# Kernel optimization log

Measured on AMD Instinct MI355X. Metric: run time of the kernel, lower is better.

Reference implementation:

```python
import jax, jax.numpy as jnp
import numpy as np

B, S, F = 16, 511, 128           # batch, input seq len, n_features
D, H, NB = 512, 8, 6             # embedding_dim, n_heads, n_blocks
DH = D // H                      # d_head
MLP = 4 * D                      # mlp_ratio=4 hard-coded in FxtBlock
OUT = 1                          # out_d
T = S + 1                        # tokens incl. cls
EPS = 1e-5                       # torch LayerNorm default eps


def pos_emb(seq_len, d):
    # matches get_positional_embeddings: sin for even j, cos for odd j (with j-1 exponent)
    i = np.arange(seq_len, dtype=np.float32)[:, None]
    j = np.arange(d)
    je = np.where(j % 2 == 0, j, j - 1).astype(np.float32)
    ang = i / (10000.0 ** (je / d))
    pe = np.where(j % 2 == 0, np.sin(ang), np.cos(ang))
    return jnp.asarray(pe, jnp.float32)


def layernorm(x, g, b):
    m = jnp.mean(x, axis=-1, keepdims=True)
    v = jnp.mean((x - m) ** 2, axis=-1, keepdims=True)
    return (x - m) * jax.lax.rsqrt(v + EPS) * g + b


def setup_inputs() -> dict:
    key = jax.random.key(0)
    ks = jax.random.split(key, 12)
    g = lambda k, shape: jax.random.normal(k, shape, jnp.float32) * 0.02
    return {
        "src": jax.random.normal(ks[0], (B, S, F), jnp.float32),
        "emb_W": g(ks[1], (F, D)), "emb_b": jnp.zeros((D,), jnp.float32),
        "cls_tok": jax.random.uniform(ks[2], (1, D), jnp.float32),
        "ln1_g": jnp.ones((NB, D), jnp.float32), "ln1_b": jnp.zeros((NB, D), jnp.float32),
        "Wq": g(ks[3], (NB, H, DH, DH)), "bq": jnp.zeros((NB, H, DH), jnp.float32),
        "Wk": g(ks[4], (NB, H, DH, DH)), "bk": jnp.zeros((NB, H, DH), jnp.float32),
        "Wv": g(ks[5], (NB, H, DH, DH)), "bv": jnp.zeros((NB, H, DH), jnp.float32),
        "ln2_g": jnp.ones((NB, D), jnp.float32), "ln2_b": jnp.zeros((NB, D), jnp.float32),
        "W1": g(ks[6], (NB, D, MLP)), "b1": jnp.zeros((NB, MLP), jnp.float32),
        "W2": g(ks[7], (NB, MLP, D)), "b2": jnp.zeros((NB, D), jnp.float32),
        "head_W": g(ks[8], (D, OUT)), "head_b": jnp.zeros((OUT,), jnp.float32),
    }


def reference(src, emb_W, emb_b, cls_tok, ln1_g, ln1_b, Wq, bq, Wk, bk, Wv, bv,
              ln2_g, ln2_b, W1, b1, W2, b2, head_W, head_b):
    b = src.shape[0]
    x = src @ emb_W + emb_b                                    # [B,S,D]
    cls = jnp.broadcast_to(cls_tok[None], (b, 1, D))
    x = jnp.concatenate([cls, x], axis=1) + pos_emb(T, D)[None]  # [B,T,D]
    scale = 1.0 / jnp.sqrt(jnp.float32(DH))
    for i in range(NB):
        h = layernorm(x, ln1_g[i], ln1_b[i])
        hh = h.reshape(b, T, H, DH)
        q = jnp.einsum('bthd,hde->bhte', hh, Wq[i]) + bq[i][None, :, None, :]
        k = jnp.einsum('bthd,hde->bhte', hh, Wk[i]) + bk[i][None, :, None, :]
        v = jnp.einsum('bthd,hde->bhte', hh, Wv[i]) + bv[i][None, :, None, :]
        attn = jax.nn.softmax(jnp.einsum('bhse,bhte->bhst', q, k) * scale, axis=-1)
        o = jnp.einsum('bhst,bhte->bhse', attn, v)             # [B,H,T,DH]
        x = x + o.transpose(0, 2, 1, 3).reshape(b, T, D)
        h2 = layernorm(x, ln2_g[i], ln2_b[i])
        x = x + (jax.nn.gelu(h2 @ W1[i] + b1[i], approximate=False) @ W2[i] + b2[i])
    return jax.nn.sigmoid(x[:, 0] @ head_W + head_b)           # [B,OUT]
```

## Files before the change

kernel.cpp:

```cpp
#include <hip/hip_runtime.h>
#include <hip/hip_bf16.h>
#include <math.h>

#define B 16
#define S 511
#define F 128
#define D 512
#define H 8
#define NB 6
#define DH 64
#define MLPD 2048
#define T 512
#define EPS 1e-5f

typedef unsigned short ushort;
typedef __attribute__((ext_vector_type(8))) short short8;
typedef __attribute__((ext_vector_type(4))) float floatx4;

__device__ __forceinline__ ushort f2bf(float f) {
    union { float f; unsigned u; } cv; cv.f = f;
    unsigned r = (cv.u + 0x7fff + ((cv.u >> 16) & 1)) >> 16;
    return (ushort)r;
}

__device__ __forceinline__ float fast_gelu(float x) {
    float z = fabsf(x) * 0.70710678118f;
    float t = 1.0f / (1.0f + 0.3275911f * z);
    float p = ((((1.061405429f * t - 1.453152027f) * t + 1.421413741f) * t
               - 0.284496736f) * t + 0.254829592f) * t;
    float erfv = 1.0f - p * __expf(-z * z);
    erfv = copysignf(erfv, x);
    return 0.5f * x * (1.0f + erfv);
}

__global__ void castsrc_kernel(const float* __restrict__ src, ushort* __restrict__ srcb) {
    int row = blockIdx.x;
    int t = row & (T - 1), b = row >> 9;
    int tid = threadIdx.x;
    ushort v = 0;
    if (t > 0) v = f2bf(src[((size_t)b * S + (t - 1)) * F + tid]);
    srcb[(size_t)row * F + tid] = v;
}

__global__ void wtrans_kernel(const float* __restrict__ W,
                              ushort* __restrict__ Wt,
                              int K, int N) {
    int kb = blockIdx.x * 32, nb = blockIdx.y * 32, mat = blockIdx.z;
    __shared__ float tile[32][33];
    int tid = threadIdx.x;
    int c = tid & 31, r0 = tid >> 5;
    const float* Wm = W + (size_t)mat * K * N;
    ushort* Wtm = Wt + (size_t)mat * K * N;
    #pragma unroll
    for (int l = 0; l < 4; ++l) {
        int r = r0 + l * 8;
        tile[r][c] = Wm[(size_t)(kb + r) * N + nb + c];
    }
    __syncthreads();
    #pragma unroll
    for (int l = 0; l < 4; ++l) {
        int r = r0 + l * 8;
        Wtm[(size_t)(nb + r) * K + kb + c] = f2bf(tile[c][r]);
    }
}

__global__ void wtransq_kernel(const float* __restrict__ Wq, const float* __restrict__ Wk,
                               const float* __restrict__ Wv,
                               ushort* __restrict__ WqT, ushort* __restrict__ WkT,
                               ushort* __restrict__ WvT) {
    int mat = blockIdx.x;
    int which = blockIdx.y;
    const float* W = (which == 0 ? Wq : which == 1 ? Wk : Wv) + (size_t)mat * 4096;
    ushort* O = (which == 0 ? WqT : which == 1 ? WkT : WvT) + (size_t)mat * 4096;
    __shared__ float t[64][65];
    int tid = threadIdx.x;
    int r0 = tid >> 6, c = tid & 63;
    #pragma unroll
    for (int l = 0; l < 16; ++l) {
        int row = r0 * 16 + l;
        t[row][c] = W[row * 64 + c];
    }
    __syncthreads();
    #pragma unroll
    for (int l = 0; l < 16; ++l) {
        int row = r0 * 16 + l;
        O[row * 64 + c] = f2bf(t[c][row]);
    }
}

__device__ __forceinline__ void gload_lds16(const ushort* g, ushort* l) {
    __builtin_amdgcn_global_load_lds((const __attribute__((address_space(1))) unsigned int*)g,
                                     (__attribute__((address_space(3))) unsigned int*)l,
                                     16, 0, 0);
}

#define S_WAITCNT_VM(N) asm volatile("s_waitcnt vmcnt(" #N ")" ::: "memory")

__global__ __launch_bounds__(256) void embed_gemm(const ushort* __restrict__ A,
                                                  const ushort* __restrict__ Bt,
                                                  const float* __restrict__ emb_b,
                                                  const float* __restrict__ cls_tok,
                                                  float* __restrict__ x) {
    __shared__ ushort As[64 * 32];
    __shared__ ushort Bs[64 * 32];
    int tid = threadIdx.x;
    int lane = tid & 63;
    int w = __builtin_amdgcn_readfirstlane(tid >> 6);
    int quad = lane >> 4, l15 = lane & 15;
    int wr = (w >> 1) * 32, wc = (w & 1) * 32;
    int m0 = blockIdx.x * 64, n0 = blockIdx.y * 64;

    floatx4 acc[2][2];
    #pragma unroll
    for (int i = 0; i < 2; ++i)
        #pragma unroll
        for (int j = 0; j < 2; ++j) acc[i][j] = (floatx4)0.f;

    int lrow = lane >> 2;
    int lk = (lane & 3) * 8;
    const ushort* Ag = A + (size_t)(m0 + 16 * w + lrow) * F + lk;
    const ushort* Bg = Bt + (size_t)(n0 + 16 * w + lrow) * F + lk;
    ushort* AsW = &As[16 * w * 32];
    ushort* BsW = &Bs[16 * w * 32];
    int fa = l15 * 32 + quad * 8;

    for (int kt = 0; kt < F; kt += 32) {
        gload_lds16(Ag + kt, AsW);
        gload_lds16(Bg + kt, BsW);
        __syncthreads();
        short8 af[2], bf[2];
        #pragma unroll
        for (int i = 0; i < 2; ++i) af[i] = *(const short8*)&As[(wr + 16 * i) * 32 + fa];
        #pragma unroll
        for (int j = 0; j < 2; ++j) bf[j] = *(const short8*)&Bs[(wc + 16 * j) * 32 + fa];
        #pragma unroll
        for (int i = 0; i < 2; ++i)
            #pragma unroll
            for (int j = 0; j < 2; ++j)
                acc[i][j] = __builtin_amdgcn_mfma_f32_16x16x32_bf16(af[i], bf[j], acc[i][j], 0, 0, 0);
        __syncthreads();
    }

    const float LOG1E4 = 9.210340371976184f;
    int rbase = (lane >> 4) * 4;
    int cidx = lane & 15;
    #pragma unroll
    for (int j = 0; j < 2; ++j) {
        int gc = n0 + wc + 16 * j + cidx;
        float je = (float)(gc & ~1);
        float freq = expf(-(je / (float)D) * LOG1E4);
        float ebv = emb_b[gc];
        float clsv = cls_tok[gc];
        bool odd = (gc & 1);
        #pragma unroll
        for (int i = 0; i < 2; ++i) {
            int gr = m0 + wr + 16 * i + rbase;
            #pragma unroll
            for (int reg = 0; reg < 4; ++reg) {
                int row = gr + reg;
                int t = row & (T - 1);
                float ang = (float)t * freq;
                float pe = odd ? cosf(ang) : sinf(ang);
                float val = (t == 0) ? (clsv + pe) : (acc[i][j][reg] + ebv + pe);
                x[(size_t)row * D + gc] = val;
            }
        }
    }
}

__global__ __launch_bounds__(256) void ln_kernel(const float* __restrict__ xin,
                                                 const float* __restrict__ g,
                                                 const float* __restrict__ bb,
                                                 ushort* __restrict__ out) {
    int lane = threadIdx.x & 63;
    int row = blockIdx.x * 4 + (threadIdx.x >> 6);
    const float* xr = xin + (size_t)row * D + lane * 8;
    float4 a0 = *(const float4*)xr;
    float4 a1 = *(const float4*)(xr + 4);
    float s = a0.x + a0.y + a0.z + a0.w + a1.x + a1.y + a1.z + a1.w;
    #pragma unroll
    for (int off = 1; off < 64; off <<= 1) s += __shfl_xor(s, off);
    float mean = s * (1.0f / (float)D);
    float d0 = a0.x - mean, d1 = a0.y - mean, d2 = a0.z - mean, d3 = a0.w - mean;
    float d4 = a1.x - mean, d5 = a1.y - mean, d6 = a1.z - mean, d7 = a1.w - mean;
    float sq = d0*d0 + d1*d1 + d2*d2 + d3*d3 + d4*d4 + d5*d5 + d6*d6 + d7*d7;
    #pragma unroll
    for (int off = 1; off < 64; off <<= 1) sq += __shfl_xor(sq, off);
    float rstd = rsqrtf(sq * (1.0f / (float)D) + EPS);
    const float* gp = g + lane * 8;
    const float* bp = bb + lane * 8;
    float4 g0 = *(const float4*)gp, g1 = *(const float4*)(gp + 4);
    float4 b0 = *(const float4*)bp, b1 = *(const float4*)(bp + 4);
    short8 o;
    o[0] = (short)f2bf(d0 * rstd * g0.x + b0.x);
    o[1] = (short)f2bf(d1 * rstd * g0.y + b0.y);
    o[2] = (short)f2bf(d2 * rstd * g0.z + b0.z);
    o[3] = (short)f2bf(d3 * rstd * g0.w + b0.w);
    o[4] = (short)f2bf(d4 * rstd * g1.x + b1.x);
    o[5] = (short)f2bf(d5 * rstd * g1.y + b1.y);
    o[6] = (short)f2bf(d6 * rstd * g1.z + b1.z);
    o[7] = (short)f2bf(d7 * rstd * g1.w + b1.w);
    *(short8*)(out + (size_t)row * D + lane * 8) = o;
}

__global__ __launch_bounds__(256) void ln_fuse_kernel(float* __restrict__ x,
                                                      const float* __restrict__ p0,
                                                      const float* __restrict__ g,
                                                      const float* __restrict__ bb,
                                                      ushort* __restrict__ out) {
    int lane = threadIdx.x & 63;
    int row = blockIdx.x * 4 + (threadIdx.x >> 6);
    size_t base = (size_t)row * D + lane * 8;
    float* xr = x + base;
    float4 a0 = *(const float4*)xr;
    float4 a1 = *(const float4*)(xr + 4);
    float4 q0 = *(const float4*)(p0 + base);
    float4 q1 = *(const float4*)(p0 + base + 4);
    a0.x += q0.x; a0.y += q0.y; a0.z += q0.z; a0.w += q0.w;
    a1.x += q1.x; a1.y += q1.y; a1.z += q1.z; a1.w += q1.w;
    *(float4*)xr = a0;
    *(float4*)(xr + 4) = a1;
    float s = a0.x + a0.y + a0.z + a0.w + a1.x + a1.y + a1.z + a1.w;
    #pragma unroll
    for (int off = 1; off < 64; off <<= 1) s += __shfl_xor(s, off);
    float mean = s * (1.0f / (float)D);
    float d0 = a0.x - mean, d1 = a0.y - mean, d2 = a0.z - mean, d3 = a0.w - mean;
    float d4 = a1.x - mean, d5 = a1.y - mean, d6 = a1.z - mean, d7 = a1.w - mean;
    float sq = d0*d0 + d1*d1 + d2*d2 + d3*d3 + d4*d4 + d5*d5 + d6*d6 + d7*d7;
    #pragma unroll
    for (int off = 1; off < 64; off <<= 1) sq += __shfl_xor(sq, off);
    float rstd = rsqrtf(sq * (1.0f / (float)D) + EPS);
    const float* gp = g + lane * 8;
    const float* bp = bb + lane * 8;
    float4 g0 = *(const float4*)gp, g1 = *(const float4*)(gp + 4);
    float4 b0 = *(const float4*)bp, b1 = *(const float4*)(bp + 4);
    short8 o;
    o[0] = (short)f2bf(d0 * rstd * g0.x + b0.x);
    o[1] = (short)f2bf(d1 * rstd * g0.y + b0.y);
    o[2] = (short)f2bf(d2 * rstd * g0.z + b0.z);
    o[3] = (short)f2bf(d3 * rstd * g0.w + b0.w);
    o[4] = (short)f2bf(d4 * rstd * g1.x + b1.x);
    o[5] = (short)f2bf(d5 * rstd * g1.y + b1.y);
    o[6] = (short)f2bf(d6 * rstd * g1.z + b1.z);
    o[7] = (short)f2bf(d7 * rstd * g1.w + b1.w);
    *(short8*)(out + (size_t)row * D + lane * 8) = o;
}

__global__ __launch_bounds__(256) void qkv_kernel(
        const ushort* __restrict__ hb,
        const ushort* __restrict__ WqT, const float* __restrict__ bq,
        const ushort* __restrict__ WkT, const float* __restrict__ bk,
        const ushort* __restrict__ WvT, const float* __restrict__ bv,
        ushort* __restrict__ qo, ushort* __restrict__ ko, ushort* __restrict__ vTo) {
    int m0 = blockIdx.x * 128;
    int hh = blockIdx.y;
    int tid = threadIdx.x;
    int lane = tid & 63;
    int w = __builtin_amdgcn_readfirstlane(tid >> 6);
    int quad = lane >> 4, l15 = lane & 15;

    short8 af[2][2];
    #pragma unroll
    for (int mt = 0; mt < 2; ++mt) {
        const ushort* ab = hb + (size_t)(m0 + w * 32 + mt * 16 + l15) * D + hh * DH + quad * 8;
        af[mt][0] = *(const short8*)(ab);
        af[mt][1] = *(const short8*)(ab + 32);
    }

    floatx4 acc[3][2][4];
    #pragma unroll
    for (int xo = 0; xo < 3; ++xo)
        #pragma unroll
        for (int mt = 0; mt < 2; ++mt)
            #pragma unroll
            for (int nt = 0; nt < 4; ++nt) acc[xo][mt][nt] = (floatx4)0.f;

    #pragma unroll
    for (int xo = 0; xo < 3; ++xo) {
        const ushort* WT = (xo == 0 ? WqT : xo == 1 ? WkT : WvT) + (size_t)hh * 4096;
        #pragma unroll
        for (int nt = 0; nt < 4; ++nt) {
            const ushort* wb = WT + (size_t)(nt * 16 + l15) * 64 + quad * 8;
            short8 bf0 = *(const short8*)(wb);
            short8 bf1 = *(const short8*)(wb + 32);
            #pragma unroll
            for (int mt = 0; mt < 2; ++mt) {
                acc[xo][mt][nt] = __builtin_amdgcn_mfma_f32_16x16x32_bf16(af[mt][0], bf0, acc[xo][mt][nt], 0, 0, 0);
                acc[xo][mt][nt] = __builtin_amdgcn_mfma_f32_16x16x32_bf16(af[mt][1], bf1, acc[xo][mt][nt], 0, 0, 0);
            }
        }
    }

    int bb = m0 >> 9;
    int bh = bb * H + hh;
    #pragma unroll
    for (int mt = 0; mt < 2; ++mt) {
        int trow = m0 + w * 32 + mt * 16 + quad * 4;
        int tt = trow & (T - 1);
        #pragma unroll
        for (int nt = 0; nt < 4; ++nt) {
            int col = nt * 16 + l15;
            float bqv = bq[hh * DH + col];
            float bkv = bk[hh * DH + col];
            float bvv = bv[hh * DH + col];
            #pragma unroll
            for (int reg = 0; reg < 4; ++reg) {
                qo[((size_t)bh * T + tt + reg) * DH + col] = f2bf(acc[0][mt][nt][reg] + bqv);
                ko[((size_t)bh * T + tt + reg) * DH + col] = f2bf(acc[1][mt][nt][reg] + bkv);
                vTo[((size_t)bh * DH + col) * T + tt + reg] = f2bf(acc[2][mt][nt][reg] + bvv);
            }
        }
    }
}

#define PSTRIDE 88
__global__ __launch_bounds__(256) void attn_kernel(const ushort* __restrict__ q,
                                                   const ushort* __restrict__ k,
                                                   const ushort* __restrict__ vT,
                                                   float* __restrict__ x) {
    int bh = blockIdx.x;
    int qt = blockIdx.y;
    int b = bh >> 3, hh = bh & 7;
    int tid = threadIdx.x;
    int lane = tid & 63;
    int w = __builtin_amdgcn_readfirstlane(tid >> 6);
    int quad = lane >> 4, l15 = lane & 15;

    __shared__ __align__(16) ushort smem[22016];
    ushort* Pw = smem + 16384 + w * (16 * PSTRIDE);

    const ushort* qbase = q + ((size_t)bh * T + qt * 64 + w * 16 + l15) * DH + quad * 8;
    short8 Qf0 = *(const short8*)(qbase);
    short8 Qf1 = *(const short8*)(qbase + 32);

    const ushort* kbase = k + (size_t)bh * T * DH;
    const ushort* vbase = vT + (size_t)bh * DH * T;

    int srow = lane >> 2;
    int scol = (lane & 3) * 8;
    const ushort* kg = kbase + (size_t)(w * 16 + srow) * DH + scol;
    const ushort* vg = vbase + (size_t)(w * 16 + srow) * T + scol;
    ushort* ldsK = smem + w * 16 * 32;
    ushort* ldsV = smem + 8192 + w * 16 * 32;

    float l_i[4] = {0.f, 0.f, 0.f, 0.f};
    floatx4 O[4];
    #pragma unroll
    for (int j = 0; j < 4; ++j) O[j] = (floatx4)0.f;

    gload_lds16(kg, ldsK);
    gload_lds16(kg + 32, ldsK + 2048);
    gload_lds16(vg, ldsV);
    gload_lds16(vg + 32, ldsV + 2048);
    __syncthreads();

    for (int kt = 0; kt < T / 64; ++kt) {
        int cur = kt & 1;
        if (kt < T / 64 - 1) {
            int nb = cur ^ 1;
            const ushort* kgn = kg + (size_t)(kt + 1) * 64 * DH;
            const ushort* vgn = vg + (kt + 1) * 64;
            gload_lds16(kgn, ldsK + nb * 4096);
            gload_lds16(kgn + 32, ldsK + nb * 4096 + 2048);
            gload_lds16(vgn, ldsV + nb * 4096);
            gload_lds16(vgn + 32, ldsV + nb * 4096 + 2048);
        }
        const ushort* Kc = smem + cur * 4096;
        const ushort* Vc = smem + 8192 + cur * 4096;

        floatx4 sc[4];
        #pragma unroll
        for (int j = 0; j < 4; ++j) {
            int ro = (j * 16 + l15) * 32 + quad * 8;
            short8 kf0 = *(const short8*)&Kc[ro];
            short8 kf1 = *(const short8*)&Kc[2048 + ro];
            floatx4 s4 = (floatx4)0.f;
            s4 = __builtin_amdgcn_mfma_f32_16x16x32_bf16(Qf0, kf0, s4, 0, 0, 0);
            s4 = __builtin_amdgcn_mfma_f32_16x16x32_bf16(Qf1, kf1, s4, 0, 0, 0);
            sc[j] = s4;
        }
        #pragma unroll
        for (int j = 0; j < 4; ++j) {
            #pragma unroll
            for (int r = 0; r < 4; ++r) {
                float p = __expf(sc[j][r] * 0.125f);
                l_i[r] += p;
                Pw[(quad * 4 + r) * PSTRIDE + j * 16 + l15] = f2bf(p);
            }
        }

        short8 af0 = *(const short8*)&Pw[l15 * PSTRIDE + quad * 8];
        short8 af1 = *(const short8*)&Pw[l15 * PSTRIDE + 32 + quad * 8];
        #pragma unroll
        for (int j = 0; j < 4; ++j) {
            int ro = (j * 16 + l15) * 32 + quad * 8;
            short8 vf0 = *(const short8*)&Vc[ro];
            short8 vf1 = *(const short8*)&Vc[2048 + ro];
            O[j] = __builtin_amdgcn_mfma_f32_16x16x32_bf16(af0, vf0, O[j], 0, 0, 0);
            O[j] = __builtin_amdgcn_mfma_f32_16x16x32_bf16(af1, vf1, O[j], 0, 0, 0);
        }
        __syncthreads();
    }

    #pragma unroll
    for (int r = 0; r < 4; ++r) {
        l_i[r] += __shfl_xor(l_i[r], 1);
        l_i[r] += __shfl_xor(l_i[r], 2);
        l_i[r] += __shfl_xor(l_i[r], 4);
        l_i[r] += __shfl_xor(l_i[r], 8);
    }

    float* Ow = (float*)smem + w * 16 * 68;
    #pragma unroll
    for (int r = 0; r < 4; ++r) {
        float rl = 1.0f / l_i[r];
        #pragma unroll
        for (int j = 0; j < 4; ++j)
            Ow[(quad * 4 + r) * 68 + j * 16 + l15] = O[j][r] * rl;
    }
    __syncthreads();
    int r4 = lane >> 4;
    int c16 = lane & 15;
    #pragma unroll
    for (int i = 0; i < 4; ++i) {
        int lrow = i * 4 + r4;
        float4 o = *(const float4*)&Ow[lrow * 68 + c16 * 4];
        int grow = qt * 64 + w * 16 + lrow;
        float* xp = &x[((size_t)(b * T) + grow) * D + hh * DH + c16 * 4];
        float4 xv = *(const float4*)xp;
        xv.x += o.x; xv.y += o.y; xv.z += o.z; xv.w += o.w;
        *(float4*)xp = xv;
    }
}

template<int BM, int EPI>
__global__ __launch_bounds__(512) void gemm_pipe(const ushort* __restrict__ A,
                                                 const ushort* __restrict__ Bt,
                                                 const float* __restrict__ bias,
                                                 void* __restrict__ Cout,
                                                 int N, int K) {
    constexpr int BN = 128;
    constexpr int BK = 64;
    constexpr int MREP = BM / 32;
    constexpr int AJ = BM / 64;
    constexpr int TILE = (BM + BN) * BK;
    __shared__ ushort lds[3 * TILE];

    int tid = threadIdx.x;
    int lane = tid & 63;
    int w = __builtin_amdgcn_readfirstlane(tid >> 6);
    int quad = lane >> 4, l15 = lane & 15;
    int wrow = (w >> 2) * (BM / 2);
    int wcol = (w & 3) * 32;
    int m0 = blockIdx.x * BM, n0 = blockIdx.y * BN;

    int lrow8 = lane >> 3;
    int lslot = lane & 7;
    int scol = (lslot ^ lrow8) * 8;
    const ushort* Asrc = A + (size_t)(m0 + w * 8 + lrow8) * K + scol;
    const ushort* Bsrc = Bt + (size_t)(n0 + w * 8 + lrow8) * K + scol;
    ushort* ldsA0 = lds + (w * 8) * BK;
    ushort* ldsB0 = lds + BM * BK + (w * 8) * BK;

    int sx0 = ((quad) ^ (l15 & 7)) * 8;
    int sx1 = ((4 + quad) ^ (l15 & 7)) * 8;

    floatx4 acc[MREP][2];
    #pragma unroll
    for (int i = 0; i < MREP; ++i) {
        acc[i][0] = (floatx4)0.f;
        acc[i][1] = (floatx4)0.f;
    }

    #define STAGE_T(t, buf) do {                                                   \
        const ushort* ap_ = Asrc + (size_t)(t) * BK;                               \
        const ushort* bp_ = Bsrc + (size_t)(t) * BK;                               \
        ushort* la_ = ldsA0 + (buf) * TILE;                                        \
        ushort* lb_ = ldsB0 + (buf) * TILE;                                        \
        _Pragma("unroll")                                                          \
        for (int j = 0; j < AJ; ++j)                                               \
            gload_lds16(ap_ + (size_t)j * 64 * K, la_ + j * 64 * BK);              \
        _Pragma("unroll")                                                          \
        for (int j = 0; j < 2; ++j)                                                \
            gload_lds16(bp_ + (size_t)j * 64 * K, lb_ + j * 64 * BK);              \
    } while (0)

    #define COMPUTE_T(buf) do {                                                    \
        const ushort* Ab_ = lds + (buf) * TILE;                                    \
        const ushort* Bb_ = Ab_ + BM * BK;                                         \
        _Pragma("unroll")                                                          \
        for (int ks = 0; ks < 2; ++ks) {                                           \
            int sx_ = ks ? sx1 : sx0;                                              \
            short8 bfr0 = *(const short8*)&Bb_[(wcol + l15) * BK + sx_];           \
            short8 bfr1 = *(const short8*)&Bb_[(wcol + 16 + l15) * BK + sx_];      \
            _Pragma("unroll")                                                      \
            for (int i = 0; i < MREP; ++i) {                                       \
                short8 af_ = *(const short8*)&Ab_[(wrow + i * 16 + l15) * BK + sx_]; \
                acc[i][0] = __builtin_amdgcn_mfma_f32_16x16x32_bf16(af_, bfr0, acc[i][0], 0, 0, 0); \
                acc[i][1] = __builtin_amdgcn_mfma_f32_16x16x32_bf16(af_, bfr1, acc[i][1], 0, 0, 0); \
            }                                                                      \
        }                                                                          \
    } while (0)

    STAGE_T(0, 0);
    STAGE_T(1, 1);

    int NT = K / BK;
    int cb = 0, nbuf = 2;
    for (int t = 0; t < NT - 2; ++t) {
        STAGE_T(t + 2, nbuf);
        if constexpr (AJ == 4) { S_WAITCNT_VM(12); } else { S_WAITCNT_VM(8); }
        __builtin_amdgcn_s_barrier();
        __builtin_amdgcn_s_setprio(1);
        COMPUTE_T(cb);
        __builtin_amdgcn_s_setprio(0);
        asm volatile("s_waitcnt lgkmcnt(0)" ::: "memory");
        __builtin_amdgcn_s_barrier();
        cb = (cb == 2) ? 0 : cb + 1;
        nbuf = (nbuf == 2) ? 0 : nbuf + 1;
    }
    if constexpr (AJ == 4) { S_WAITCNT_VM(6); } else { S_WAITCNT_VM(4); }
    __builtin_amdgcn_s_barrier();
    __builtin_amdgcn_s_setprio(1);
    COMPUTE_T(cb);
    __builtin_amdgcn_s_setprio(0);
    asm volatile("s_waitcnt lgkmcnt(0)" ::: "memory");
    __builtin_amdgcn_s_barrier();
    cb = (cb == 2) ? 0 : cb + 1;
    S_WAITCNT_VM(0);
    __builtin_amdgcn_s_barrier();
    COMPUTE_T(cb);

    #undef STAGE_T
    #undef COMPUTE_T

    int rbase = quad * 4;
    #pragma unroll
    for (int i = 0; i < MREP; ++i) {
        #pragma unroll
        for (int n = 0; n < 2; ++n) {
            int gc = n0 + wcol + n * 16 + l15;
            float bv = bias[gc];
            int gr = m0 + wrow + i * 16 + rbase;
            #pragma unroll
            for (int reg = 0; reg < 4; ++reg) {
                if constexpr (EPI == 0) {
                    ((ushort*)Cout)[(size_t)(gr + reg) * N + gc] =
                        f2bf(fast_gelu(acc[i][n][reg] + bv));
                } else {
                    ((float*)Cout)[(size_t)(gr + reg) * N + gc] = acc[i][n][reg] + bv;
                }
            }
        }
    }
}

__global__ __launch_bounds__(256) void ln_cls_kernel(const float* __restrict__ x,
                                                     const float* __restrict__ g,
                                                     const float* __restrict__ bb,
                                                     ushort* __restrict__ h2c) {
    int lane = threadIdx.x & 63;
    int r = blockIdx.x * 4 + (threadIdx.x >> 6);
    const float* xr = x + (size_t)r * T * D + lane * 8;
    float4 a0 = *(const float4*)xr;
    float4 a1 = *(const float4*)(xr + 4);
    float s = a0.x + a0.y + a0.z + a0.w + a1.x + a1.y + a1.z + a1.w;
    #pragma unroll
    for (int off = 1; off < 64; off <<= 1) s += __shfl_xor(s, off);
    float mean = s * (1.0f / (float)D);
    float d0 = a0.x - mean, d1 = a0.y - mean, d2 = a0.z - mean, d3 = a0.w - mean;
    float d4 = a1.x - mean, d5 = a1.y - mean, d6 = a1.z - mean, d7 = a1.w - mean;
    float sq = d0*d0 + d1*d1 + d2*d2 + d3*d3 + d4*d4 + d5*d5 + d6*d6 + d7*d7;
    #pragma unroll
    for (int off = 1; off < 64; off <<= 1) sq += __shfl_xor(sq, off);
    float rstd = rsqrtf(sq * (1.0f / (float)D) + EPS);
    const float* gp = g + lane * 8;
    const float* bp = bb + lane * 8;
    float4 g0 = *(const float4*)gp, g1 = *(const float4*)(gp + 4);
    float4 b0 = *(const float4*)bp, b1v = *(const float4*)(bp + 4);
    short8 o;
    o[0] = (short)f2bf(d0 * rstd * g0.x + b0.x);
    o[1] = (short)f2bf(d1 * rstd * g0.y + b0.y);
    o[2] = (short)f2bf(d2 * rstd * g0.z + b0.z);
    o[3] = (short)f2bf(d3 * rstd * g0.w + b0.w);
    o[4] = (short)f2bf(d4 * rstd * g1.x + b1v.x);
    o[5] = (short)f2bf(d5 * rstd * g1.y + b1v.y);
    o[6] = (short)f2bf(d6 * rstd * g1.z + b1v.z);
    o[7] = (short)f2bf(d7 * rstd * g1.w + b1v.w);
    *(short8*)(h2c + r * D + lane * 8) = o;
}

__global__ __launch_bounds__(256) void gemm1_cls(const ushort* __restrict__ h2c,
                                                 const ushort* __restrict__ W1t,
                                                 const float* __restrict__ b1,
                                                 ushort* __restrict__ uc) {
    int tid = threadIdx.x;
    int lane = tid & 63;
    int w = __builtin_amdgcn_readfirstlane(tid >> 6);
    int quad = lane >> 4, l15 = lane & 15;
    int nb = blockIdx.x * 64 + w * 16;

    short8 af[16];
    #pragma unroll
    for (int ks = 0; ks < 16; ++ks)
        af[ks] = *(const short8*)&h2c[l15 * D + ks * 32 + quad * 8];

    const ushort* wrow = W1t + (size_t)(nb + l15) * D + quad * 8;
    floatx4 acc = (floatx4)0.f;
    #pragma unroll
    for (int ks = 0; ks < 16; ++ks) {
        short8 bf = *(const short8*)(wrow + ks * 32);
        acc = __builtin_amdgcn_mfma_f32_16x16x32_bf16(af[ks], bf, acc, 0, 0, 0);
    }
    float bv = b1[nb + l15];
    #pragma unroll
    for (int reg = 0; reg < 4; ++reg)
        uc[(size_t)(quad * 4 + reg) * MLPD + nb + l15] = f2bf(fast_gelu(acc[reg] + bv));
}

__global__ __launch_bounds__(256) void gemm2_cls(const ushort* __restrict__ uc,
                                                 const ushort* __restrict__ W2t,
                                                 const float* __restrict__ b2,
                                                 float* __restrict__ p0) {
    __shared__ float red[4 * 256];
    int tid = threadIdx.x;
    int lane = tid & 63;
    int w = __builtin_amdgcn_readfirstlane(tid >> 6);
    int quad = lane >> 4, l15 = lane & 15;
    int nb = blockIdx.x * 16;

    const ushort* wrow = W2t + (size_t)(nb + l15) * MLPD + quad * 8;
    floatx4 acc = (floatx4)0.f;
    #pragma unroll
    for (int k8 = 0; k8 < 16; ++k8) {
        int ks = w * 16 + k8;
        short8 a2 = *(const short8*)&uc[(size_t)l15 * MLPD + ks * 32 + quad * 8];
        short8 bf = *(const short8*)(wrow + (size_t)ks * 32);
        acc = __builtin_amdgcn_mfma_f32_16x16x32_bf16(a2, bf, acc, 0, 0, 0);
    }
    #pragma unroll
    for (int reg = 0; reg < 4; ++reg)
        red[w * 256 + (quad * 4 + reg) * 16 + l15] = acc[reg];
    __syncthreads();
    int row = tid >> 4, col = tid & 15;
    float s = red[row * 16 + col] + red[256 + row * 16 + col]
            + red[512 + row * 16 + col] + red[768 + row * 16 + col];
    p0[((size_t)row * T) * D + nb + col] = s + b2[nb + col];
}

__global__ void head_kernel(const float* __restrict__ x,
                            const float* __restrict__ p0,
                            const float* __restrict__ hw,
                            const float* __restrict__ hb,
                            float* __restrict__ out) {
    int b = blockIdx.x;
    int tid = threadIdx.x;
    size_t idx = (size_t)b * T * D + tid;
    float s = (x[idx] + p0[idx]) * hw[tid];
    #pragma unroll
    for (int off = 32; off > 0; off >>= 1) s += __shfl_down(s, off, 64);
    __shared__ float red[8];
    if ((tid & 63) == 0) red[tid >> 6] = s;
    __syncthreads();
    if (tid == 0) {
        float t = 0.f;
        #pragma unroll
        for (int i = 0; i < 8; ++i) t += red[i];
        out[b] = 1.0f / (1.0f + __expf(-(t + hb[0])));
    }
}

extern "C" void kernel_launch(void* const* d_in, const int* in_sizes, int n_in,
                              void* d_out, int out_size, void* d_ws, size_t ws_size,
                              hipStream_t stream) {
    const float* src     = (const float*)d_in[0];
    const float* emb_W   = (const float*)d_in[1];
    const float* emb_b   = (const float*)d_in[2];
    const float* cls_tok = (const float*)d_in[3];
    const float* ln1_g   = (const float*)d_in[4];
    const float* ln1_b   = (const float*)d_in[5];
    const float* Wq      = (const float*)d_in[6];
    const float* bq      = (const float*)d_in[7];
    const float* Wk      = (const float*)d_in[8];
    const float* bk      = (const float*)d_in[9];
    const float* Wv      = (const float*)d_in[10];
    const float* bv      = (const float*)d_in[11];
    const float* ln2_g   = (const float*)d_in[12];
    const float* ln2_b   = (const float*)d_in[13];
    const float* W1      = (const float*)d_in[14];
    const float* b1      = (const float*)d_in[15];
    const float* W2      = (const float*)d_in[16];
    const float* b2      = (const float*)d_in[17];
    const float* head_W  = (const float*)d_in[18];
    const float* head_b  = (const float*)d_in[19];

    const size_t NTOK = (size_t)B * T;
    char* wsb = (char*)d_ws;
    float*  x    = (float*)wsb;      wsb += NTOK * D * 4;
    float*  p0   = (float*)wsb;      wsb += NTOK * D * 4;
    ushort* hbuf = (ushort*)wsb;     wsb += NTOK * D * 2;
    ushort* q    = (ushort*)wsb;     wsb += NTOK * D * 2;
    ushort* k    = (ushort*)wsb;     wsb += NTOK * D * 2;
    ushort* vT   = (ushort*)wsb;     wsb += NTOK * D * 2;
    ushort* u    = (ushort*)wsb;     wsb += NTOK * MLPD * 2;
    ushort* W1t  = (ushort*)wsb;     wsb += (size_t)NB * D * MLPD * 2;
    ushort* W2t  = (ushort*)wsb;     wsb += (size_t)NB * D * MLPD * 2;
    ushort* WqT  = (ushort*)wsb;     wsb += (size_t)NB * H * DH * DH * 2;
    ushort* WkT  = (ushort*)wsb;     wsb += (size_t)NB * H * DH * DH * 2;
    ushort* WvT  = (ushort*)wsb;     wsb += (size_t)NB * H * DH * DH * 2;
    ushort* srcb = (ushort*)wsb;     wsb += NTOK * F * 2;
    ushort* embWt= (ushort*)wsb;     wsb += (size_t)F * D * 2;
    ushort* h2c  = (ushort*)wsb;     wsb += (size_t)16 * D * 2;
    ushort* ucls = (ushort*)wsb;     wsb += (size_t)16 * MLPD * 2;

    wtrans_kernel<<<dim3(D / 32, MLPD / 32, NB), 256, 0, stream>>>(W1, W1t, D, MLPD);
    wtrans_kernel<<<dim3(MLPD / 32, D / 32, NB), 256, 0, stream>>>(W2, W2t, MLPD, D);
    wtransq_kernel<<<dim3(NB * H, 3), 256, 0, stream>>>(Wq, Wk, Wv, WqT, WkT, WvT);
    wtrans_kernel<<<dim3(F / 32, D / 32, 1), 256, 0, stream>>>(emb_W, embWt, F, D);
    castsrc_kernel<<<B * T, F, 0, stream>>>(src, srcb);

    embed_gemm<<<dim3(B * T / 64, D / 64), 256, 0, stream>>>(srcb, embWt, emb_b, cls_tok, x);

    for (int i = 0; i < NB; ++i) {
        if (i == 0)
            ln_kernel<<<B * T / 4, 256, 0, stream>>>(x, ln1_g, ln1_b, hbuf);
        else
            ln_fuse_kernel<<<B * T / 4, 256, 0, stream>>>(x, p0,
                ln1_g + i * D, ln1_b + i * D, hbuf);
        qkv_kernel<<<dim3(B * T / 128, H), 256, 0, stream>>>(hbuf,
            WqT + (size_t)i * H * DH * DH, bq + (size_t)i * H * DH,
            WkT + (size_t)i * H * DH * DH, bk + (size_t)i * H * DH,
            WvT + (size_t)i * H * DH * DH, bv + (size_t)i * H * DH,
            q, k, vT);
        if (i < NB - 1) {
            attn_kernel<<<dim3(B * H, T / 64), 256, 0, stream>>>(q, k, vT, x);
            ln_kernel<<<B * T / 4, 256, 0, stream>>>(x, ln2_g + i * D, ln2_b + i * D, hbuf);
            gemm_pipe<256, 0><<<dim3(B * T / 256, MLPD / 128), 512, 0, stream>>>(
                hbuf, W1t + (size_t)i * D * MLPD, b1 + (size_t)i * MLPD, u, MLPD, D);
            gemm_pipe<128, 1><<<dim3(B * T / 128, D / 128), 512, 0, stream>>>(
                u, W2t + (size_t)i * MLPD * D, b2 + (size_t)i * D, p0, D, MLPD);
        } else {
            attn_kernel<<<dim3(B * H, 1), 256, 0, stream>>>(q, k, vT, x);
            ln_cls_kernel<<<4, 256, 0, stream>>>(x,
                ln2_g + (size_t)i * D, ln2_b + (size_t)i * D, h2c);
            gemm1_cls<<<MLPD / 64, 256, 0, stream>>>(h2c,
                W1t + (size_t)i * D * MLPD, b1 + (size_t)i * MLPD, ucls);
            gemm2_cls<<<D / 16, 256, 0, stream>>>(ucls,
                W2t + (size_t)i * MLPD * D, b2 + (size_t)i * D, p0);
            head_kernel<<<B, 512, 0, stream>>>(x, p0, head_W, head_b, (float*)d_out);
        }
    }
}
```

Measured before the change: 773.9 us.

## Fuse LayerNorm into QKV projection and residual add into MLP down-projection

The first LayerNorm is merged into the QKV kernel. Each block normalizes 32 rows into LDS, and each wave then computes two heads, so the bf16 hidden buffer no longer goes through global memory. The second MLP GEMM now adds its output directly into x through a read-modify-write epilogue, which removes the separate p0 buffer and the residual pass inside the LayerNorm kernel. Attention MFMA sections also get s_setprio hints. The trade-offs are fewer QKV blocks (256 instead of 512), heavier per-block work, and an extra read of x in the GEMM epilogue.

After: 762.3 us. No clear change (-1.5%).

```diff
diff --git a/kernel.cpp b/kernel.cpp
--- a/kernel.cpp
+++ b/kernel.cpp
@@ -203,111 +203,105 @@
     *(short8*)(out + (size_t)row * D + lane * 8) = o;
 }
 
-__global__ __launch_bounds__(256) void ln_fuse_kernel(float* __restrict__ x,
-                                                      const float* __restrict__ p0,
-                                                      const float* __restrict__ g,
-                                                      const float* __restrict__ bb,
-                                                      ushort* __restrict__ out) {
-    int lane = threadIdx.x & 63;
-    int row = blockIdx.x * 4 + (threadIdx.x >> 6);
-    size_t base = (size_t)row * D + lane * 8;
-    float* xr = x + base;
-    float4 a0 = *(const float4*)xr;
-    float4 a1 = *(const float4*)(xr + 4);
-    float4 q0 = *(const float4*)(p0 + base);
-    float4 q1 = *(const float4*)(p0 + base + 4);
-    a0.x += q0.x; a0.y += q0.y; a0.z += q0.z; a0.w += q0.w;
-    a1.x += q1.x; a1.y += q1.y; a1.z += q1.z; a1.w += q1.w;
-    *(float4*)xr = a0;
-    *(float4*)(xr + 4) = a1;
-    float s = a0.x + a0.y + a0.z + a0.w + a1.x + a1.y + a1.z + a1.w;
-    #pragma unroll
-    for (int off = 1; off < 64; off <<= 1) s += __shfl_xor(s, off);
-    float mean = s * (1.0f / (float)D);
-    float d0 = a0.x - mean, d1 = a0.y - mean, d2 = a0.z - mean, d3 = a0.w - mean;
-    float d4 = a1.x - mean, d5 = a1.y - mean, d6 = a1.z - mean, d7 = a1.w - mean;
-    float sq = d0*d0 + d1*d1 + d2*d2 + d3*d3 + d4*d4 + d5*d5 + d6*d6 + d7*d7;
-    #pragma unroll
-    for (int off = 1; off < 64; off <<= 1) sq += __shfl_xor(sq, off);
-    float rstd = rsqrtf(sq * (1.0f / (float)D) + EPS);
-    const float* gp = g + lane * 8;
-    const float* bp = bb + lane * 8;
-    float4 g0 = *(const float4*)gp, g1 = *(const float4*)(gp + 4);
-    float4 b0 = *(const float4*)bp, b1 = *(const float4*)(bp + 4);
-    short8 o;
-    o[0] = (short)f2bf(d0 * rstd * g0.x + b0.x);
-    o[1] = (short)f2bf(d1 * rstd * g0.y + b0.y);
-    o[2] = (short)f2bf(d2 * rstd * g0.z + b0.z);
-    o[3] = (short)f2bf(d3 * rstd * g0.w + b0.w);
-    o[4] = (short)f2bf(d4 * rstd * g1.x + b1.x);
-    o[5] = (short)f2bf(d5 * rstd * g1.y + b1.y);
-    o[6] = (short)f2bf(d6 * rstd * g1.z + b1.z);
-    o[7] = (short)f2bf(d7 * rstd * g1.w + b1.w);
-    *(short8*)(out + (size_t)row * D + lane * 8) = o;
-}
-
-__global__ __launch_bounds__(256) void qkv_kernel(
-        const ushort* __restrict__ hb,
+#define LQPAD 520
+__global__ __launch_bounds__(256) void lnqkv_kernel(
+        const float* __restrict__ x,
+        const float* __restrict__ g, const float* __restrict__ bb,
         const ushort* __restrict__ WqT, const float* __restrict__ bq,
         const ushort* __restrict__ WkT, const float* __restrict__ bk,
         const ushort* __restrict__ WvT, const float* __restrict__ bv,
         ushort* __restrict__ qo, ushort* __restrict__ ko, ushort* __restrict__ vTo) {
-    int m0 = blockIdx.x * 128;
-    int hh = blockIdx.y;
+    __shared__ ushort hl[32 * LQPAD];
     int tid = threadIdx.x;
     int lane = tid & 63;
     int w = __builtin_amdgcn_readfirstlane(tid >> 6);
     int quad = lane >> 4, l15 = lane & 15;
-
-    short8 af[2][2];
-    #pragma unroll
-    for (int mt = 0; mt < 2; ++mt) {
-        const ushort* ab = hb + (size_t)(m0 + w * 32 + mt * 16 + l15) * D + hh * DH + quad * 8;
-        af[mt][0] = *(const short8*)(ab);
-        af[mt][1] = *(const short8*)(ab + 32);
-    }
-
-    floatx4 acc[3][2][4];
-    #pragma unroll
-    for (int xo = 0; xo < 3; ++xo)
+    int m0 = blockIdx.x * 32;
+
+    for (int it = 0; it < 8; ++it) {
+        int lr = it * 4 + w;
+        const float* xr = x + (size_t)(m0 + lr) * D + lane * 8;
+        float4 a0 = *(const float4*)xr;
+        float4 a1 = *(const float4*)(xr + 4);
+        float s = a0.x + a0.y + a0.z + a0.w + a1.x + a1.y + a1.z + a1.w;
+        #pragma unroll
+        for (int off = 1; off < 64; off <<= 1) s += __shfl_xor(s, off);
+        float mean = s * (1.0f / (float)D);
+        float d0 = a0.x - mean, d1 = a0.y - mean, d2 = a0.z - mean, d3 = a0.w - mean;
+        float d4 = a1.x - mean, d5 = a1.y - mean, d6 = a1.z - mean, d7 = a1.w - mean;
+        float sq = d0*d0 + d1*d1 + d2*d2 + d3*d3 + d4*d4 + d5*d5 + d6*d6 + d7*d7;
+        #pragma unroll
+        for (int off = 1; off < 64; off <<= 1) sq += __shfl_xor(sq, off);
+        float rstd = rsqrtf(sq * (1.0f / (float)D) + EPS);
+        const float* gp = g + lane * 8;
+        const float* bp = bb + lane * 8;
+        float4 g0 = *(const float4*)gp, g1 = *(const float4*)(gp + 4);
+        float4 b0 = *(const float4*)bp, b1v = *(const float4*)(bp + 4);
+        short8 o;
+        o[0] = (short)f2bf(d0 * rstd * g0.x + b0.x);
+        o[1] = (short)f2bf(d1 * rstd * g0.y + b0.y);
+        o[2] = (short)f2bf(d2 * rstd * g0.z + b0.z);
+        o[3] = (short)f2bf(d3 * rstd * g0.w + b0.w);
+        o[4] = (short)f2bf(d4 * rstd * g1.x + b1v.x);
+        o[5] = (short)f2bf(d5 * rstd * g1.y + b1v.y);
+        o[6] = (short)f2bf(d6 * rstd * g1.z + b1v.z);
+        o[7] = (short)f2bf(d7 * rstd * g1.w + b1v.w);
+        *(short8*)(hl + lr * LQPAD + lane * 8) = o;
+    }
+    __syncthreads();
+
+    int bb_ = m0 >> 9;
+    #pragma unroll
+    for (int hp = 0; hp < 2; ++hp) {
+        int hh = w * 2 + hp;
+        short8 af[2][2];
         #pragma unroll
         for (int mt = 0; mt < 2; ++mt)
             #pragma unroll
-            for (int nt = 0; nt < 4; ++nt) acc[xo][mt][nt] = (floatx4)0.f;
-
-    #pragma unroll
-    for (int xo = 0; xo < 3; ++xo) {
-        const ushort* WT = (xo == 0 ? WqT : xo == 1 ? WkT : WvT) + (size_t)hh * 4096;
-        #pragma unroll
-        for (int nt = 0; nt < 4; ++nt) {
-            const ushort* wb = WT + (size_t)(nt * 16 + l15) * 64 + quad * 8;
-            short8 bf0 = *(const short8*)(wb);
-            short8 bf1 = *(const short8*)(wb + 32);
+            for (int ks = 0; ks < 2; ++ks)
+                af[mt][ks] = *(const short8*)&hl[(mt * 16 + l15) * LQPAD + hh * DH + ks * 32 + quad * 8];
+
+        floatx4 acc[3][2][4];
+        #pragma unroll
+        for (int xo = 0; xo < 3; ++xo)
             #pragma unroll
-            for (int mt = 0; mt < 2; ++mt) {
-                acc[xo][mt][nt] = __builtin_amdgcn_mfma_f32_16x16x32_bf16(af[mt][0], bf0, acc[xo][mt][nt], 0, 0, 0);
-                acc[xo][mt][nt] = __builtin_amdgcn_mfma_f32_16x16x32_bf16(af[mt][1], bf1, acc[xo][mt][nt], 0, 0, 0);
+            for (int mt = 0; mt < 2; ++mt)
+                #pragma unroll
+                for (int nt = 0; nt < 4; ++nt) acc[xo][mt][nt] = (floatx4)0.f;
+
+        #pragma unroll
+        for (int xo = 0; xo < 3; ++xo) {
+            const ushort* WT = (xo == 0 ? WqT : xo == 1 ? WkT : WvT) + (size_t)hh * 4096;
+            #pragma unroll
+            for (int nt = 0; nt < 4; ++nt) {
+                const ushort* wb = WT + (size_t)(nt * 16 + l15) * 64 + quad * 8;
+                short8 bf0 = *(const short8*)(wb);
+                short8 bf1 = *(const short8*)(wb + 32);
+                #pragma unroll
+                for (int mt = 0; mt < 2; ++mt) {
+                    acc[xo][mt][nt] = __builtin_amdgcn_mfma_f32_16x16x32_bf16(af[mt][0], bf0, acc[xo][mt][nt], 0, 0, 0);
+                    acc[xo][mt][nt] = __builtin_amdgcn_mfma_f32_16x16x32_bf16(af[mt][1], bf1, acc[xo][mt][nt], 0, 0, 0);
+                }
             }
         }
-    }
-
-    int bb = m0 >> 9;
-    int bh = bb * H + hh;
-    #pragma unroll
-    for (int mt = 0; mt < 2; ++mt) {
-        int trow = m0 + w * 32 + mt * 16 + quad * 4;
-        int tt = trow & (T - 1);
-        #pragma unroll
-        for (int nt = 0; nt < 4; ++nt) {
-            int col = nt * 16 + l15;
-            float bqv = bq[hh * DH + col];
-            float bkv = bk[hh * DH + col];
-            float bvv = bv[hh * DH + col];
+
+        int bh = bb_ * H + hh;
+        #pragma unroll
+        for (int mt = 0; mt < 2; ++mt) {
+            int trow = m0 + mt * 16 + quad * 4;
+            int tt = trow & (T - 1);
             #pragma unroll
-            for (int reg = 0; reg < 4; ++reg) {
-                qo[((size_t)bh * T + tt + reg) * DH + col] = f2bf(acc[0][mt][nt][reg] + bqv);
-                ko[((size_t)bh * T + tt + reg) * DH + col] = f2bf(acc[1][mt][nt][reg] + bkv);
-                vTo[((size_t)bh * DH + col) * T + tt + reg] = f2bf(acc[2][mt][nt][reg] + bvv);
+            for (int nt = 0; nt < 4; ++nt) {
+                int col = nt * 16 + l15;
+                float bqv = bq[hh * DH + col];
+                float bkv = bk[hh * DH + col];
+                float bvv = bv[hh * DH + col];
+                #pragma unroll
+                for (int reg = 0; reg < 4; ++reg) {
+                    qo[((size_t)bh * T + tt + reg) * DH + col] = f2bf(acc[0][mt][nt][reg] + bqv);
+                    ko[((size_t)bh * T + tt + reg) * DH + col] = f2bf(acc[1][mt][nt][reg] + bkv);
+                    vTo[((size_t)bh * DH + col) * T + tt + reg] = f2bf(acc[2][mt][nt][reg] + bvv);
+                }
             }
         }
     }
@@ -369,6 +363,7 @@
         const ushort* Vc = smem + 8192 + cur * 4096;
 
         floatx4 sc[4];
+        __builtin_amdgcn_s_setprio(1);
         #pragma unroll
         for (int j = 0; j < 4; ++j) {
             int ro = (j * 16 + l15) * 32 + quad * 8;
@@ -379,6 +374,7 @@
             s4 = __builtin_amdgcn_mfma_f32_16x16x32_bf16(Qf1, kf1, s4, 0, 0, 0);
             sc[j] = s4;
         }
+        __builtin_amdgcn_s_setprio(0);
         #pragma unroll
         for (int j = 0; j < 4; ++j) {
             #pragma unroll
@@ -391,6 +387,7 @@
 
         short8 af0 = *(const short8*)&Pw[l15 * PSTRIDE + quad * 8];
         short8 af1 = *(const short8*)&Pw[l15 * PSTRIDE + 32 + quad * 8];
+        __builtin_amdgcn_s_setprio(1);
         #pragma unroll
         for (int j = 0; j < 4; ++j) {
             int ro = (j * 16 + l15) * 32 + quad * 8;
@@ -399,6 +396,7 @@
             O[j] = __builtin_amdgcn_mfma_f32_16x16x32_bf16(af0, vf0, O[j], 0, 0, 0);
             O[j] = __builtin_amdgcn_mfma_f32_16x16x32_bf16(af1, vf1, O[j], 0, 0, 0);
         }
+        __builtin_amdgcn_s_setprio(0);
         __syncthreads();
     }
 
@@ -547,8 +545,11 @@
                 if constexpr (EPI == 0) {
                     ((ushort*)Cout)[(size_t)(gr + reg) * N + gc] =
                         f2bf(fast_gelu(acc[i][n][reg] + bv));
+                } else if constexpr (EPI == 1) {
+                    ((float*)Cout)[(size_t)(gr + reg) * N + gc] = acc[i][n][reg] + bv;
                 } else {
-                    ((float*)Cout)[(size_t)(gr + reg) * N + gc] = acc[i][n][reg] + bv;
+                    float* xp = (float*)Cout + (size_t)(gr + reg) * N + gc;
+                    *xp = *xp + acc[i][n][reg] + bv;
                 }
             }
         }
@@ -621,7 +622,7 @@
 __global__ __launch_bounds__(256) void gemm2_cls(const ushort* __restrict__ uc,
                                                  const ushort* __restrict__ W2t,
                                                  const float* __restrict__ b2,
-                                                 float* __restrict__ p0) {
+                                                 float* __restrict__ p0c) {
     __shared__ float red[4 * 256];
     int tid = threadIdx.x;
     int lane = tid & 63;
@@ -645,18 +646,17 @@
     int row = tid >> 4, col = tid & 15;
     float s = red[row * 16 + col] + red[256 + row * 16 + col]
             + red[512 + row * 16 + col] + red[768 + row * 16 + col];
-    p0[((size_t)row * T) * D + nb + col] = s + b2[nb + col];
+    p0c[(size_t)row * D + nb + col] = s + b2[nb + col];
 }
 
 __global__ void head_kernel(const float* __restrict__ x,
-                            const float* __restrict__ p0,
+                            const float* __restrict__ p0c,
                             const float* __restrict__ hw,
                             const float* __restrict__ hb,
                             float* __restrict__ out) {
     int b = blockIdx.x;
     int tid = threadIdx.x;
-    size_t idx = (size_t)b * T * D + tid;
-    float s = (x[idx] + p0[idx]) * hw[tid];
+    float s = (x[(size_t)b * T * D + tid] + p0c[(size_t)b * D + tid]) * hw[tid];
     #pragma unroll
     for (int off = 32; off > 0; off >>= 1) s += __shfl_down(s, off, 64);
     __shared__ float red[8];
@@ -697,7 +697,6 @@
     const size_t NTOK = (size_t)B * T;
     char* wsb = (char*)d_ws;
     float*  x    = (float*)wsb;      wsb += NTOK * D * 4;
-    float*  p0   = (float*)wsb;      wsb += NTOK * D * 4;
     ushort* hbuf = (ushort*)wsb;     wsb += NTOK * D * 2;
     ushort* q    = (ushort*)wsb;     wsb += NTOK * D * 2;
     ushort* k    = (ushort*)wsb;     wsb += NTOK * D * 2;
@@ -712,6 +711,7 @@
     ushort* embWt= (ushort*)wsb;     wsb += (size_t)F * D * 2;
     ushort* h2c  = (ushort*)wsb;     wsb += (size_t)16 * D * 2;
     ushort* ucls = (ushort*)wsb;     wsb += (size_t)16 * MLPD * 2;
+    float*  p0c  = (float*)wsb;      wsb += (size_t)16 * D * 4;
 
     wtrans_kernel<<<dim3(D / 32, MLPD / 32, NB), 256, 0, stream>>>(W1, W1t, D, MLPD);
     wtrans_kernel<<<dim3(MLPD / 32, D / 32, NB), 256, 0, stream>>>(W2, W2t, MLPD, D);
@@ -722,12 +722,8 @@
     embed_gemm<<<dim3(B * T / 64, D / 64), 256, 0, stream>>>(srcb, embWt, emb_b, cls_tok, x);
 
     for (int i = 0; i < NB; ++i) {
-        if (i == 0)
-            ln_kernel<<<B * T / 4, 256, 0, stream>>>(x, ln1_g, ln1_b, hbuf);
-        else
-            ln_fuse_kernel<<<B * T / 4, 256, 0, stream>>>(x, p0,
-                ln1_g + i * D, ln1_b + i * D, hbuf);
-        qkv_kernel<<<dim3(B * T / 128, H), 256, 0, stream>>>(hbuf,
+        lnqkv_kernel<<<B * T / 32, 256, 0, stream>>>(x,
+            ln1_g + i * D, ln1_b + i * D,
             WqT + (size_t)i * H * DH * DH, bq + (size_t)i * H * DH,
             WkT + (size_t)i * H * DH * DH, bk + (size_t)i * H * DH,
             WvT + (size_t)i * H * DH * DH, bv + (size_t)i * H * DH,
@@ -737,8 +733,8 @@
             ln_kernel<<<B * T / 4, 256, 0, stream>>>(x, ln2_g + i * D, ln2_b + i * D, hbuf);
             gemm_pipe<256, 0><<<dim3(B * T / 256, MLPD / 128), 512, 0, stream>>>(
                 hbuf, W1t + (size_t)i * D * MLPD, b1 + (size_t)i * MLPD, u, MLPD, D);
-            gemm_pipe<128, 1><<<dim3(B * T / 128, D / 128), 512, 0, stream>>>(
-                u, W2t + (size_t)i * MLPD * D, b2 + (size_t)i * D, p0, D, MLPD);
+            gemm_pipe<128, 2><<<dim3(B * T / 128, D / 128), 512, 0, stream>>>(
+                u, W2t + (size_t)i * MLPD * D, b2 + (size_t)i * D, x, D, MLPD);
         } else {
             attn_kernel<<<dim3(B * H, 1), 256, 0, stream>>>(q, k, vT, x);
             ln_cls_kernel<<<4, 256, 0, stream>>>(x,
@@ -746,8 +742,8 @@
             gemm1_cls<<<MLPD / 64, 256, 0, stream>>>(h2c,
                 W1t + (size_t)i * D * MLPD, b1 + (size_t)i * MLPD, ucls);
             gemm2_cls<<<D / 16, 256, 0, stream>>>(ucls,
-                W2t + (size_t)i * MLPD * D, b2 + (size_t)i * D, p0);
-            head_kernel<<<B, 512, 0, stream>>>(x, p0, head_W, head_b, (float*)d_out);
-        }
-    }
-}
+                W2t + (size_t)i * MLPD * D, b2 + (size_t)i * D, p0c);
+            head_kernel<<<B, 512, 0, stream>>>(x, p0c, head_W, head_b, (float*)d_out);
+        }
+    }
+}
```
